# Performance work log

Measured on AMD Instinct MI355X. Metric: run time of the kernel, lower is better.

## Reference

```python
import jax, jax.numpy as jnp
import numpy as np

EMBED_DIM = 1024
N_HEADS = 16
HEAD_DIM = EMBED_DIM // N_HEADS


def setup_inputs() -> dict:
    key = jax.random.key(0)
    k_x, k_qw, k_qb, k_ow, k_ob = jax.random.split(key, 5)
    s = 1.0 / np.sqrt(EMBED_DIM)
    return {
        "x": jax.random.normal(k_x, (2, 2048, EMBED_DIM), dtype=jnp.float32),
        "qkv_w": jax.random.uniform(k_qw, (3 * EMBED_DIM, EMBED_DIM), jnp.float32, -s, s),
        "qkv_b": jax.random.uniform(k_qb, (3 * EMBED_DIM,), jnp.float32, -s, s),
        "out_w": jax.random.uniform(k_ow, (EMBED_DIM, EMBED_DIM), jnp.float32, -s, s),
        "out_b": jax.random.uniform(k_ob, (EMBED_DIM,), jnp.float32, -s, s),
    }


def reference(x, qkv_w, qkv_b, out_w, out_b):
    B, S, E = x.shape
    # fused QKV projection (torch Linear: x @ W^T + b)
    qkv = x @ qkv_w.T + qkv_b                      # [B,S,3E]
    qkv = qkv.reshape(B, S, N_HEADS, 3 * HEAD_DIM).transpose(0, 2, 1, 3)  # [B,H,S,3d]
    q, k, v = jnp.split(qkv, 3, axis=-1)           # each [B,H,S,d]
    scores = jnp.einsum("bhqd,bhkd->bhqk", q, k) / jnp.sqrt(jnp.float32(HEAD_DIM))
    weights = jax.nn.softmax(scores, axis=-1)      # [B,H,S,S]
    attn = jnp.einsum("bhqk,bhkd->bhqd", weights, v)
    attn = attn.transpose(0, 2, 1, 3).reshape(B, S, E)
    return attn @ out_w.T + out_b
```

## Files before the change

### kernel.cpp

```cpp
#include <hip/hip_runtime.h>
#include <hip/hip_bf16.h>


#define E_DIM   1024
#define NHEADS  16
#define HDIM    64
#define SEQ     2048
#define TOK     4096
#define QKV_DIM 3072
#define QK_STRIDE 2048
#define QSCALE_F 0.18033688011112042f

typedef __attribute__((ext_vector_type(8))) short bf16x8;
typedef __attribute__((ext_vector_type(4))) float f32x4;
typedef __attribute__((ext_vector_type(4))) int   i32x4;
typedef __attribute__((ext_vector_type(2))) int   i32x2;
typedef __attribute__((ext_vector_type(2))) __bf16 bf16x2_t;

#if __has_builtin(__builtin_amdgcn_exp2f)
#define EXP2F(x) __builtin_amdgcn_exp2f(x)
#else
#define EXP2F(x) exp2f(x)
#endif

__device__ __forceinline__ unsigned pack2bf(float a, float b) {
#if __has_builtin(__builtin_amdgcn_cvt_pk_bf16_f32)
    union { bf16x2_t v; unsigned u; } u;
    u.v = __builtin_amdgcn_cvt_pk_bf16_f32(a, b);
    return u.u;
#else
    union { float f; unsigned u; } ua, ub; ua.f = a; ub.f = b;
    unsigned ra = ua.u + 0x7FFF + ((ua.u >> 16) & 1);
    unsigned rb = ub.u + 0x7FFF + ((ub.u >> 16) & 1);
    return (ra >> 16) | (rb & 0xFFFF0000u);
#endif
}

__device__ __forceinline__ unsigned short f2bf(float x) {
    return (unsigned short)(pack2bf(x, x) & 0xFFFFu);
}

__device__ __forceinline__ void load_lds16(const void* g, void* l) {
    __builtin_amdgcn_global_load_lds(
        (const __attribute__((address_space(1))) void*)g,
        (__attribute__((address_space(3))) void*)l, 16, 0, 0);
}

__device__ __forceinline__ bf16x8 lds_read8(const unsigned short* p) {
    union { i32x4 i; bf16x8 b; } u;
    u.i = *(const i32x4*)p;
    return u.b;
}

__device__ __forceinline__ f32x4 mfma16(bf16x8 a, bf16x8 b, f32x4 c) {
    return __builtin_amdgcn_mfma_f32_16x16x32_bf16(a, b, c, 0, 0, 0);
}

__global__ void cast3_kernel(const float* __restrict__ a, unsigned short* __restrict__ oa, int na4,
                             const float* __restrict__ b, unsigned short* __restrict__ ob, int nb4,
                             const float* __restrict__ c, unsigned short* __restrict__ oc) {
    int i = blockIdx.x * blockDim.x + threadIdx.x;
    const float* src; unsigned short* dst; int j;
    if (i < na4)            { src = a; dst = oa; j = i; }
    else if (i < na4 + nb4) { src = b; dst = ob; j = i - na4; }
    else                    { src = c; dst = oc; j = i - na4 - nb4; }
    f32x4 v = ((const f32x4*)src)[j];
    union { i32x2 i2; unsigned u[2]; } o;
    o.u[0] = pack2bf(v.x, v.y);
    o.u[1] = pack2bf(v.z, v.w);
    ((i32x2*)dst)[j] = o.i2;
}

__global__ __launch_bounds__(256, 3)
void gemm_qkv_kernel(const unsigned short* __restrict__ A,
                     const unsigned short* __restrict__ B,
                     const float* __restrict__ bias,
                     unsigned short* __restrict__ qk,
                     unsigned short* __restrict__ vT,
                     int K) {
    __shared__ __align__(16) unsigned short As[128 * 64];
    __shared__ __align__(16) unsigned short Bs[128 * 64];

    const int tid  = threadIdx.x;
    const int wave = tid >> 6, lane = tid & 63;
    const int quad = lane >> 4, l16 = lane & 15;
    const int row0 = blockIdx.y * 128, col0 = blockIdx.x * 128;
    const int wr = (wave >> 1) * 64, wc = (wave & 1) * 64;

    f32x4 acc[4][4];
#pragma unroll
    for (int i = 0; i < 4; ++i)
#pragma unroll
        for (int j = 0; j < 4; ++j) acc[i][j] = (f32x4){0.f, 0.f, 0.f, 0.f};

    const int nkt = K >> 6;
    for (int kt = 0; kt < nkt; ++kt) {
        const int k0 = kt << 6;
#pragma unroll
        for (int i = 0; i < 4; ++i) {
            int p = i * 256 + tid;
            int r = p >> 3;
            int kc = (p & 7) ^ (r & 7);
            load_lds16(A + (size_t)(row0 + r) * K + k0 + kc * 8, &As[p * 8]);
        }
#pragma unroll
        for (int i = 0; i < 4; ++i) {
            int p = i * 256 + tid;
            int r = p >> 3;
            int kc = (p & 7) ^ (r & 7);
            load_lds16(B + (size_t)(col0 + r) * K + k0 + kc * 8, &Bs[p * 8]);
        }
        __syncthreads();

#pragma unroll
        for (int ks = 0; ks < 2; ++ks) {
            bf16x8 af[4], bfr[4];
#pragma unroll
            for (int rb = 0; rb < 4; ++rb) {
                int r_l  = wr + rb * 16 + l16;
                int phys = (ks * 4 + quad) ^ (l16 & 7);
                af[rb] = lds_read8(&As[r_l * 64 + phys * 8]);
            }
#pragma unroll
            for (int cb = 0; cb < 4; ++cb) {
                int r_l  = wc + cb * 16 + l16;
                int phys = (ks * 4 + quad) ^ (l16 & 7);
                bfr[cb] = lds_read8(&Bs[r_l * 64 + phys * 8]);
            }
#pragma unroll
            for (int rb = 0; rb < 4; ++rb)
#pragma unroll
                for (int cb = 0; cb < 4; ++cb)
                    acc[rb][cb] = mfma16(af[rb], bfr[cb], acc[rb][cb]);
        }
        __syncthreads();
    }

#pragma unroll
    for (int rb = 0; rb < 4; ++rb)
#pragma unroll
        for (int cb = 0; cb < 4; ++cb) {
            int col = col0 + wc + cb * 16 + l16;
            int h    = col / 192;
            int part = col - h * 192;
            float bv = bias[col];
            int row_b = row0 + wr + rb * 16 + quad * 4;
            float v[4];
#pragma unroll
            for (int reg = 0; reg < 4; ++reg) v[reg] = acc[rb][cb][reg] + bv;
            if (part < 128) {
                float sc = (part < 64) ? QSCALE_F : 1.0f;
                size_t base = (size_t)h * 128 + part;
#pragma unroll
                for (int reg = 0; reg < 4; ++reg)
                    qk[(size_t)(row_b + reg) * QK_STRIDE + base] = f2bf(v[reg] * sc);
            } else {
                int i  = part - 128;
                int b  = row_b >> 11;
                int s  = row_b & 2047;
                i32x2 pk;
                pk.x = (int)pack2bf(v[0], v[1]);
                pk.y = (int)pack2bf(v[2], v[3]);
                *(i32x2*)&vT[(((size_t)(b * 16 + h)) * 64 + i) * SEQ + s] = pk;
            }
        }
}

__global__ __launch_bounds__(256, 2)
void gemm2_kernel(const unsigned short* __restrict__ A,
                  const unsigned short* __restrict__ B,
                  const float* __restrict__ bias,
                  float* __restrict__ C, int M, int N, int K) {
    __shared__ __align__(16) unsigned short As[128 * 64];
    __shared__ __align__(16) unsigned short Bs[64 * 64];

    const int tid  = threadIdx.x;
    const int wave = tid >> 6, lane = tid & 63;
    const int quad = lane >> 4, l16 = lane & 15;
    const int row0 = blockIdx.y * 128, col0 = blockIdx.x * 64;
    const int wr = wave * 32;

    f32x4 acc[2][4];
#pragma unroll
    for (int i = 0; i < 2; ++i)
#pragma unroll
        for (int j = 0; j < 4; ++j) acc[i][j] = (f32x4){0.f, 0.f, 0.f, 0.f};

    const int nkt = K >> 6;
    for (int kt = 0; kt < nkt; ++kt) {
        const int k0 = kt << 6;
#pragma unroll
        for (int i = 0; i < 4; ++i) {
            int p = i * 256 + tid;
            int r = p >> 3;
            int kc = (p & 7) ^ (r & 7);
            load_lds16(A + (size_t)(row0 + r) * K + k0 + kc * 8, &As[p * 8]);
        }
#pragma unroll
        for (int i = 0; i < 2; ++i) {
            int p = i * 256 + tid;
            int r = p >> 3;
            int kc = (p & 7) ^ (r & 7);
            load_lds16(B + (size_t)(col0 + r) * K + k0 + kc * 8, &Bs[p * 8]);
        }
        __syncthreads();

#pragma unroll
        for (int ks = 0; ks < 2; ++ks) {
            bf16x8 af[2], bfr[4];
#pragma unroll
            for (int rb = 0; rb < 2; ++rb) {
                int r_l  = wr + rb * 16 + l16;
                int phys = (ks * 4 + quad) ^ (l16 & 7);
                af[rb] = lds_read8(&As[r_l * 64 + phys * 8]);
            }
#pragma unroll
            for (int cb = 0; cb < 4; ++cb) {
                int r_l  = cb * 16 + l16;
                int phys = (ks * 4 + quad) ^ (l16 & 7);
                bfr[cb] = lds_read8(&Bs[r_l * 64 + phys * 8]);
            }
#pragma unroll
            for (int rb = 0; rb < 2; ++rb)
#pragma unroll
                for (int cb = 0; cb < 4; ++cb)
                    acc[rb][cb] = mfma16(af[rb], bfr[cb], acc[rb][cb]);
        }
        __syncthreads();
    }

#pragma unroll
    for (int rb = 0; rb < 2; ++rb)
#pragma unroll
        for (int cb = 0; cb < 4; ++cb) {
            int col = col0 + cb * 16 + l16;
            float bv = bias[col];
#pragma unroll
            for (int reg = 0; reg < 4; ++reg) {
                int row = row0 + wr + rb * 16 + quad * 4 + reg;
                C[(size_t)row * N + col] = acc[rb][cb][reg] + bv;
            }
        }
}

__global__ __launch_bounds__(512, 4)
void attn_kernel(const unsigned short* __restrict__ qk,
                 const unsigned short* __restrict__ vT,
                 unsigned short* __restrict__ attn) {
    __shared__ __align__(16) unsigned short Ks[128 * 64];
    __shared__ __align__(16) unsigned short Vs[64 * 128];
    __shared__ __align__(16) unsigned short Ps[8][16 * 64];

    const int tid  = threadIdx.x;
    const int wave = tid >> 6, lane = tid & 63;
    const int quad = lane >> 4, l16 = lane & 15;
    const int bh = blockIdx.y;
    const int b = bh >> 4, h = bh & 15;
    const int q0 = blockIdx.x * 128;
    const size_t rowbase = (size_t)b * SEQ;
    const int qtok = q0 + wave * 16 + l16;

    const int sw3 = l16 & 7;
    const unsigned short* Kb0 = &Ks[l16 * 64 + ((quad ^ sw3) * 8)];
    const unsigned short* Kb1 = &Ks[l16 * 64 + (((4 + quad) ^ sw3) * 8)];
    const unsigned short* Vb[4] = {
        &Vs[l16 * 128 + (((0 * 4 + quad) ^ l16) * 8)],
        &Vs[l16 * 128 + (((1 * 4 + quad) ^ l16) * 8)],
        &Vs[l16 * 128 + (((2 * 4 + quad) ^ l16) * 8)],
        &Vs[l16 * 128 + (((3 * 4 + quad) ^ l16) * 8)] };
    unsigned short* Pw[4];
#pragma unroll
    for (int c4 = 0; c4 < 4; ++c4)
        Pw[c4] = &Ps[wave][l16 * 64 + (((c4 * 2 + (quad >> 1)) ^ sw3) * 8) + (quad & 1) * 4];
    const unsigned short* Pr0 = &Ps[wave][l16 * 64 + ((quad ^ sw3) * 8)];
    const unsigned short* Pr1 = &Ps[wave][l16 * 64 + (((4 + quad) ^ sw3) * 8)];

    bf16x8 qf[2];
#pragma unroll
    for (int ks = 0; ks < 2; ++ks) {
        const unsigned short* p =
            qk + (rowbase + qtok) * QK_STRIDE + h * 128 + ks * 32 + quad * 8;
        union { i32x4 i; bf16x8 b; } u;
        u.i = *(const i32x4*)p;
        qf[ks] = u.b;
    }

    f32x4 o[4];
#pragma unroll
    for (int ib = 0; ib < 4; ++ib) o[ib] = (f32x4){0.f, 0.f, 0.f, 0.f};
    float l_s = 0.f;

    for (int kt = 0; kt < SEQ / 128; ++kt) {
        const int kb = kt * 128;
        const unsigned short* kbase = qk + (rowbase + kb) * QK_STRIDE + h * 128 + 64;
        const unsigned short* vbase = vT + (size_t)bh * 64 * SEQ + kb;
#pragma unroll
        for (int i = 0; i < 2; ++i) {
            int p = i * 512 + tid;
            int r = p >> 3;
            int kc = (p & 7) ^ (r & 7);
            load_lds16(kbase + r * QK_STRIDE + kc * 8, &Ks[p * 8]);
        }
#pragma unroll
        for (int i = 0; i < 2; ++i) {
            int p = i * 512 + tid;
            int r = p >> 4;
            int c = (p & 15) ^ (r & 15);
            load_lds16(vbase + r * SEQ + c * 8, &Vs[p * 8]);
        }
        __syncthreads();

        f32x4 s[8];
#pragma unroll
        for (int cb = 0; cb < 8; ++cb) s[cb] = (f32x4){0.f, 0.f, 0.f, 0.f};
#pragma unroll
        for (int cb = 0; cb < 8; ++cb) {
            bf16x8 kf0 = lds_read8(Kb0 + cb * 1024);
            s[cb] = mfma16(kf0, qf[0], s[cb]);
        }
#pragma unroll
        for (int cb = 0; cb < 8; ++cb) {
            bf16x8 kf1 = lds_read8(Kb1 + cb * 1024);
            s[cb] = mfma16(kf1, qf[1], s[cb]);
        }

        float rs = 0.f;
#pragma unroll
        for (int cb = 0; cb < 8; ++cb)
#pragma unroll
            for (int r = 0; r < 4; ++r) {
                float pv = EXP2F(s[cb][r]);
                s[cb][r] = pv;
                rs += pv;
            }
        rs += __shfl_xor(rs, 16);
        rs += __shfl_xor(rs, 32);
        l_s += rs;

#pragma unroll
        for (int half = 0; half < 2; ++half) {
#pragma unroll
            for (int c4 = 0; c4 < 4; ++c4) {
                int cb = half * 4 + c4;
                i32x2 pk;
                pk.x = (int)pack2bf(s[cb][0], s[cb][1]);
                pk.y = (int)pack2bf(s[cb][2], s[cb][3]);
                *(i32x2*)Pw[c4] = pk;
            }
            __asm__ volatile("s_waitcnt lgkmcnt(0)" ::: "memory");
            {
                bf16x8 pf0 = lds_read8(Pr0);
#pragma unroll
                for (int ib = 0; ib < 4; ++ib) {
                    bf16x8 vf = lds_read8(Vb[half * 2 + 0] + ib * 2048);
                    o[ib] = mfma16(pf0, vf, o[ib]);
                }
                bf16x8 pf1 = lds_read8(Pr1);
#pragma unroll
                for (int ib = 0; ib < 4; ++ib) {
                    bf16x8 vf = lds_read8(Vb[half * 2 + 1] + ib * 2048);
                    o[ib] = mfma16(pf1, vf, o[ib]);
                }
            }
        }
        __syncthreads();
    }

    float il[4];
#pragma unroll
    for (int r = 0; r < 4; ++r) il[r] = 1.0f / __shfl(l_s, quad * 4 + r);
#pragma unroll
    for (int ib = 0; ib < 4; ++ib)
#pragma unroll
        for (int r = 0; r < 4; ++r) {
            int t = q0 + wave * 16 + quad * 4 + r;
            attn[(rowbase + t) * E_DIM + h * 64 + ib * 16 + l16] =
                f2bf(o[ib][r] * il[r]);
        }
}

extern "C" void kernel_launch(void* const* d_in, const int* in_sizes, int n_in,
                              void* d_out, int out_size, void* d_ws, size_t ws_size,
                              hipStream_t stream) {
    const float* x     = (const float*)d_in[0];
    const float* qkv_w = (const float*)d_in[1];
    const float* qkv_b = (const float*)d_in[2];
    const float* out_w = (const float*)d_in[3];
    const float* out_b = (const float*)d_in[4];

    char* ws = (char*)d_ws;
    unsigned short* xb   = (unsigned short*)(ws);
    unsigned short* wqkv = (unsigned short*)(ws + 8388608);
    unsigned short* wout = (unsigned short*)(ws + 14680064);
    unsigned short* qk   = (unsigned short*)(ws + 16777216);
    unsigned short* attn = (unsigned short*)(ws + 33554432);
    unsigned short* vT   = (unsigned short*)(ws + 41943040);

    cast3_kernel<<<8192, 256, 0, stream>>>(x, xb, 1048576,
                                           qkv_w, wqkv, 786432,
                                           out_w, wout);

    gemm_qkv_kernel<<<dim3(24, 32), 256, 0, stream>>>(
        xb, wqkv, qkv_b, qk, vT, E_DIM);

    attn_kernel<<<dim3(16, 32), 512, 0, stream>>>(qk, vT, attn);

    gemm2_kernel<<<dim3(16, 32), 256, 0, stream>>>(
        attn, wout, out_b, (float*)d_out, TOK, E_DIM, E_DIM);
}
```

Measured before the change: 184.1 us.

## Double-buffer K/V tiles in attention and shrink blocks to 64 queries

The attention kernel now uses 256-thread blocks covering 64 query rows each, with 64-key tiles instead of 128, and a grid that is twice as large. K and V tiles are double-buffered in a single LDS array, so the next tile's async loads are issued before computing on the current tile, which drops one barrier per iteration. This is meant to hide global-to-LDS latency and raise occupancy, at the cost of more iterations and more blocks re-reading the same K/V data.

```diff
diff --git a/kernel.cpp b/kernel.cpp
--- a/kernel.cpp
+++ b/kernel.cpp
@@ -243,37 +243,42 @@
         }
 }
 
-__global__ __launch_bounds__(512, 4)
+__global__ __launch_bounds__(256, 4)
 void attn_kernel(const unsigned short* __restrict__ qk,
                  const unsigned short* __restrict__ vT,
                  unsigned short* __restrict__ attn) {
-    __shared__ __align__(16) unsigned short Ks[128 * 64];
-    __shared__ __align__(16) unsigned short Vs[64 * 128];
-    __shared__ __align__(16) unsigned short Ps[8][16 * 64];
+    __shared__ __align__(16) unsigned short lds[20480];
 
     const int tid  = threadIdx.x;
     const int wave = tid >> 6, lane = tid & 63;
     const int quad = lane >> 4, l16 = lane & 15;
     const int bh = blockIdx.y;
     const int b = bh >> 4, h = bh & 15;
-    const int q0 = blockIdx.x * 128;
+    const int q0 = blockIdx.x * 64;
     const size_t rowbase = (size_t)b * SEQ;
     const int qtok = q0 + wave * 16 + l16;
-
     const int sw3 = l16 & 7;
-    const unsigned short* Kb0 = &Ks[l16 * 64 + ((quad ^ sw3) * 8)];
-    const unsigned short* Kb1 = &Ks[l16 * 64 + (((4 + quad) ^ sw3) * 8)];
-    const unsigned short* Vb[4] = {
-        &Vs[l16 * 128 + (((0 * 4 + quad) ^ l16) * 8)],
-        &Vs[l16 * 128 + (((1 * 4 + quad) ^ l16) * 8)],
-        &Vs[l16 * 128 + (((2 * 4 + quad) ^ l16) * 8)],
-        &Vs[l16 * 128 + (((3 * 4 + quad) ^ l16) * 8)] };
-    unsigned short* Pw[4];
+
+    const unsigned short* kroot = qk + rowbase * QK_STRIDE + h * 128 + 64;
+    const unsigned short* vroot = vT + (size_t)bh * 64 * SEQ;
+
+    int srow[2], scol[2];
+#pragma unroll
+    for (int i = 0; i < 2; ++i) {
+        int p = i * 256 + tid;
+        srow[i] = p >> 3;
+        scol[i] = ((p & 7) ^ (srow[i] & 7)) * 8;
+    }
+
+    const int fO0 = l16 * 64 + ((quad ^ sw3) * 8);
+    const int fO1 = l16 * 64 + (((4 + quad) ^ sw3) * 8);
+    int pwO[4];
 #pragma unroll
     for (int c4 = 0; c4 < 4; ++c4)
-        Pw[c4] = &Ps[wave][l16 * 64 + (((c4 * 2 + (quad >> 1)) ^ sw3) * 8) + (quad & 1) * 4];
-    const unsigned short* Pr0 = &Ps[wave][l16 * 64 + ((quad ^ sw3) * 8)];
-    const unsigned short* Pr1 = &Ps[wave][l16 * 64 + (((4 + quad) ^ sw3) * 8)];
+        pwO[c4] = 16384 + wave * 1024 + l16 * 64
+                + (((c4 * 2 + (quad >> 1)) ^ sw3) * 8) + (quad & 1) * 4;
+    const int prO0 = 16384 + wave * 1024 + fO0;
+    const int prO1 = 16384 + wave * 1024 + fO1;
 
     bf16x8 qf[2];
 #pragma unroll
@@ -290,43 +295,58 @@
     for (int ib = 0; ib < 4; ++ib) o[ib] = (f32x4){0.f, 0.f, 0.f, 0.f};
     float l_s = 0.f;
 
-    for (int kt = 0; kt < SEQ / 128; ++kt) {
-        const int kb = kt * 128;
-        const unsigned short* kbase = qk + (rowbase + kb) * QK_STRIDE + h * 128 + 64;
-        const unsigned short* vbase = vT + (size_t)bh * 64 * SEQ + kb;
-#pragma unroll
-        for (int i = 0; i < 2; ++i) {
-            int p = i * 512 + tid;
-            int r = p >> 3;
-            int kc = (p & 7) ^ (r & 7);
-            load_lds16(kbase + r * QK_STRIDE + kc * 8, &Ks[p * 8]);
-        }
-#pragma unroll
-        for (int i = 0; i < 2; ++i) {
-            int p = i * 512 + tid;
-            int r = p >> 4;
-            int c = (p & 15) ^ (r & 15);
-            load_lds16(vbase + r * SEQ + c * 8, &Vs[p * 8]);
-        }
+#pragma unroll
+    for (int i = 0; i < 2; ++i) {
+        int p = i * 256 + tid;
+        load_lds16(kroot + srow[i] * QK_STRIDE + scol[i], &lds[p * 8]);
+    }
+#pragma unroll
+    for (int i = 0; i < 2; ++i) {
+        int p = i * 256 + tid;
+        load_lds16(vroot + srow[i] * SEQ + scol[i], &lds[8192 + p * 8]);
+    }
+
+    for (int kt = 0; kt < SEQ / 64; ++kt) {
+        const int cur = kt & 1;
         __syncthreads();
 
-        f32x4 s[8];
-#pragma unroll
-        for (int cb = 0; cb < 8; ++cb) s[cb] = (f32x4){0.f, 0.f, 0.f, 0.f};
-#pragma unroll
-        for (int cb = 0; cb < 8; ++cb) {
-            bf16x8 kf0 = lds_read8(Kb0 + cb * 1024);
-            s[cb] = mfma16(kf0, qf[0], s[cb]);
-        }
-#pragma unroll
-        for (int cb = 0; cb < 8; ++cb) {
-            bf16x8 kf1 = lds_read8(Kb1 + cb * 1024);
-            s[cb] = mfma16(kf1, qf[1], s[cb]);
+        if (kt < SEQ / 64 - 1) {
+            const int kb = (kt + 1) * 64;
+            const int nb = (cur ^ 1) * 4096;
+#pragma unroll
+            for (int i = 0; i < 2; ++i) {
+                int p = i * 256 + tid;
+                load_lds16(kroot + (size_t)(kb + srow[i]) * QK_STRIDE + scol[i],
+                           &lds[nb + p * 8]);
+            }
+#pragma unroll
+            for (int i = 0; i < 2; ++i) {
+                int p = i * 256 + tid;
+                load_lds16(vroot + srow[i] * SEQ + kb + scol[i],
+                           &lds[8192 + nb + p * 8]);
+            }
+        }
+
+        const unsigned short* ksb = &lds[cur * 4096];
+        const unsigned short* vsb = &lds[8192 + cur * 4096];
+
+        f32x4 s[4];
+#pragma unroll
+        for (int cb = 0; cb < 4; ++cb) s[cb] = (f32x4){0.f, 0.f, 0.f, 0.f};
+#pragma unroll
+        for (int cb = 0; cb < 4; ++cb) {
+            bf16x8 kf = lds_read8(ksb + fO0 + cb * 1024);
+            s[cb] = mfma16(kf, qf[0], s[cb]);
+        }
+#pragma unroll
+        for (int cb = 0; cb < 4; ++cb) {
+            bf16x8 kf = lds_read8(ksb + fO1 + cb * 1024);
+            s[cb] = mfma16(kf, qf[1], s[cb]);
         }
 
         float rs = 0.f;
 #pragma unroll
-        for (int cb = 0; cb < 8; ++cb)
+        for (int cb = 0; cb < 4; ++cb)
 #pragma unroll
             for (int r = 0; r < 4; ++r) {
                 float pv = EXP2F(s[cb][r]);
@@ -338,32 +358,27 @@
         l_s += rs;
 
 #pragma unroll
-        for (int half = 0; half < 2; ++half) {
-#pragma unroll
-            for (int c4 = 0; c4 < 4; ++c4) {
-                int cb = half * 4 + c4;
-                i32x2 pk;
-                pk.x = (int)pack2bf(s[cb][0], s[cb][1]);
-                pk.y = (int)pack2bf(s[cb][2], s[cb][3]);
-                *(i32x2*)Pw[c4] = pk;
-            }
-            __asm__ volatile("s_waitcnt lgkmcnt(0)" ::: "memory");
-            {
-                bf16x8 pf0 = lds_read8(Pr0);
-#pragma unroll
-                for (int ib = 0; ib < 4; ++ib) {
-                    bf16x8 vf = lds_read8(Vb[half * 2 + 0] + ib * 2048);
-                    o[ib] = mfma16(pf0, vf, o[ib]);
-                }
-                bf16x8 pf1 = lds_read8(Pr1);
-#pragma unroll
-                for (int ib = 0; ib < 4; ++ib) {
-                    bf16x8 vf = lds_read8(Vb[half * 2 + 1] + ib * 2048);
-                    o[ib] = mfma16(pf1, vf, o[ib]);
-                }
-            }
-        }
-        __syncthreads();
+        for (int c4 = 0; c4 < 4; ++c4) {
+            i32x2 pk;
+            pk.x = (int)pack2bf(s[c4][0], s[c4][1]);
+            pk.y = (int)pack2bf(s[c4][2], s[c4][3]);
+            *(i32x2*)&lds[pwO[c4]] = pk;
+        }
+        __asm__ volatile("s_waitcnt lgkmcnt(0)" ::: "memory");
+        {
+            bf16x8 pf0 = lds_read8(&lds[prO0]);
+#pragma unroll
+            for (int ib = 0; ib < 4; ++ib) {
+                bf16x8 vf = lds_read8(vsb + fO0 + ib * 1024);
+                o[ib] = mfma16(pf0, vf, o[ib]);
+            }
+            bf16x8 pf1 = lds_read8(&lds[prO1]);
+#pragma unroll
+            for (int ib = 0; ib < 4; ++ib) {
+                bf16x8 vf = lds_read8(vsb + fO1 + ib * 1024);
+                o[ib] = mfma16(pf1, vf, o[ib]);
+            }
+        }
     }
 
     float il[4];
@@ -403,7 +418,7 @@
     gemm_qkv_kernel<<<dim3(24, 32), 256, 0, stream>>>(
         xb, wqkv, qkv_b, qk, vT, E_DIM);
 
-    attn_kernel<<<dim3(16, 32), 512, 0, stream>>>(qk, vT, attn);
+    attn_kernel<<<dim3(32, 32), 256, 0, stream>>>(qk, vT, attn);
 
     gemm2_kernel<<<dim3(16, 32), 256, 0, stream>>>(
         attn, wout, out_b, (float*)d_out, TOK, E_DIM, E_DIM);
```

Measured after the change: 188.8 us. 2.6% more time.
